# Optimization experiments

Hardware: AMD Instinct MI355X
Metric: run time of the kernel (lower is better)

## Reference

```python
import jax, jax.numpy as jnp
import numpy as np


def ternarize_weight(w):
    # abs-mean threshold quantization to {-am, 0, +am}
    abs_mean = jnp.maximum(jnp.abs(w).mean(), 1e-5)
    thr = 0.7 * abs_mean
    q = jnp.where(w > thr, 1.0, jnp.where(w < -thr, -1.0, 0.0))
    # STE: forward value is q*abs_mean, grad flows to w as identity
    return w + jax.lax.stop_gradient(q * abs_mean - w)


def rotate_half(x):
    x1, x2 = jnp.split(x, 2, axis=-1)
    return jnp.concatenate([-x2, x1], axis=-1)


def setup_inputs() -> dict:
    key = jax.random.key(0)
    k1, k2, k3, k4, k5 = jax.random.split(key, 5)
    B, T, C, H = 2, 2048, 1024, 16
    D = C // H
    x = jax.random.normal(k1, (B, T, C), dtype=jnp.float32)
    cos = jax.random.uniform(k2, (1, 1, T, D), dtype=jnp.float32)
    sin = jax.random.uniform(k3, (1, 1, T, D), dtype=jnp.float32)
    w_qkv = jax.random.normal(k4, (3 * C, C), dtype=jnp.float32) / np.sqrt(C)
    w_proj = jax.random.normal(k5, (C, C), dtype=jnp.float32) / np.sqrt(C)
    return {"x": x, "cos": cos, "sin": sin, "w_qkv": w_qkv, "w_proj": w_proj}


def reference(x, cos, sin, w_qkv, w_proj):
    B, T, C = x.shape
    H = 16
    D = C // H
    wq = ternarize_weight(w_qkv)
    wp = ternarize_weight(w_proj)
    qkv = x @ wq.T  # [B,T,3C]
    q, k, v = jnp.split(qkv, 3, axis=-1)
    # [B,T,C] -> [B,H,T,D]
    q = q.reshape(B, T, H, D).transpose(0, 2, 1, 3)
    k = k.reshape(B, T, H, D).transpose(0, 2, 1, 3)
    v = v.reshape(B, T, H, D).transpose(0, 2, 1, 3)
    # RoPE
    q = q * cos + rotate_half(q) * sin
    k = k * cos + rotate_half(k) * sin
    # causal SDPA
    scale = 1.0 / np.sqrt(D)
    scores = jnp.einsum("bhqd,bhkd->bhqk", q, k) * scale
    causal = jnp.tril(jnp.ones((T, T), dtype=bool))
    scores = jnp.where(causal, scores, jnp.finfo(scores.dtype).min)
    attn = jax.nn.softmax(scores, axis=-1)
    y = jnp.einsum("bhqk,bhkd->bhqd", attn, v)  # [B,H,T,D]
    y = y.transpose(0, 2, 1, 3).reshape(B, T, C)
    return y @ wp.T
```

## Files before the change

### kernel.cpp

```cpp
#include <hip/hip_runtime.h>
#include <hip/hip_bf16.h>

#define B_ 2
#define T_ 2048
#define C_ 1024
#define H_ 16
#define D_ 64
#define M_ 4096
#define N3C 3072

using short8  = __attribute__((ext_vector_type(8))) short;
using floatx4 = __attribute__((ext_vector_type(4))) float;
typedef unsigned int u32;

__device__ __forceinline__ unsigned short f2b(float f) {
  __hip_bfloat16 h = __float2bfloat16(f);
  return *reinterpret_cast<unsigned short*>(&h);
}
__device__ __forceinline__ float b2f(unsigned short u) {
  union { unsigned int i; float f; } x; x.i = ((unsigned int)u) << 16; return x.f;
}
__device__ __forceinline__ u32 pk2(float a, float b) {
  float2 t; t.x = a; t.y = b;
  __hip_bfloat162 p = __float22bfloat162_rn(t);
  return *reinterpret_cast<u32*>(&p);
}

#if __has_builtin(__builtin_amdgcn_exp2f)
__device__ __forceinline__ float ex2(float x) { return __builtin_amdgcn_exp2f(x); }
#else
__device__ __forceinline__ float ex2(float x) { return exp2f(x); }
#endif

__device__ __forceinline__ void gll16(const void* g, void* l) {
  __builtin_amdgcn_global_load_lds((const __attribute__((address_space(1))) u32*)g,
                                   (__attribute__((address_space(3))) u32*)l, 16, 0, 0);
}

#define SYNCV(N) do {                                                   \
    asm volatile("s_waitcnt vmcnt(" #N ")" ::: "memory");               \
    __builtin_amdgcn_s_barrier();                                       \
    asm volatile("" ::: "memory");                                      \
  } while (0)


__global__ void abs_sum2(const float* __restrict__ wq, const float* __restrict__ wp,
                         double* __restrict__ sums) {
  __shared__ double red[4];
  const float* w = blockIdx.y ? wp : wq;
  const int n4 = blockIdx.y ? (C_ * C_ / 4) : (3 * C_ * C_ / 4);
  int stride = gridDim.x * blockDim.x;
  double s = 0.0;
  for (int i = blockIdx.x * blockDim.x + threadIdx.x; i < n4; i += stride) {
    float4 v = ((const float4*)w)[i];
    s += (double)fabsf(v.x) + (double)fabsf(v.y) + (double)fabsf(v.z) + (double)fabsf(v.w);
  }
  #pragma unroll
  for (int off = 32; off > 0; off >>= 1)
    s += __shfl_down(s, off, 64);
  if ((threadIdx.x & 63) == 0) red[threadIdx.x >> 6] = s;
  __syncthreads();
  if (threadIdx.x == 0) atomicAdd(sums + blockIdx.y, (red[0] + red[1]) + (red[2] + red[3]));
}

__global__ void tern_cvt(const float* __restrict__ wq, const float* __restrict__ wp,
                         const float* __restrict__ x,
                         unsigned short* __restrict__ oq, unsigned short* __restrict__ op,
                         unsigned short* __restrict__ xb,
                         const double* __restrict__ sums, float* __restrict__ ams) {
  const int NQ = 3 * C_ * C_;
  const int NP = C_ * C_;
  int i = blockIdx.x * blockDim.x + threadIdx.x;
  float am0 = fmaxf((float)(sums[0] * (1.0 / NQ)), 1e-5f);
  float am1 = fmaxf((float)(sums[1] * (1.0 / NP)), 1e-5f);
  if (i == 0) { ams[0] = am0; ams[1] = am1; }
  if (i < NQ) {
    float thr = 0.7f * am0, v = wq[i];
    oq[i] = (v > thr) ? 0x3F80u : ((v < -thr) ? 0xBF80u : 0u);
  } else if (i < NQ + NP) {
    int j = i - NQ;
    float thr = 0.7f * am1, v = wp[j];
    op[j] = (v > thr) ? 0x3F80u : ((v < -thr) ? 0xBF80u : 0u);
  } else {
    int j = i - NQ - NP;
    float4 v = ((const float4*)x)[j];
    ushort4 o; o.x = f2b(v.x); o.y = f2b(v.y); o.z = f2b(v.z); o.w = f2b(v.w);
    ((ushort4*)xb)[j] = o;
  }
}


__global__ __launch_bounds__(256) void gemm_qkv(const unsigned short* __restrict__ A,
                                                const unsigned short* __restrict__ W,
                                                const float* __restrict__ scale_ptr,
                                                const float* __restrict__ cosp,
                                                const float* __restrict__ sinp,
                                                unsigned short* __restrict__ Qb,
                                                unsigned short* __restrict__ Kb,
                                                unsigned short* __restrict__ Vtb) {
  const int K = C_;
  __shared__ __attribute__((aligned(16))) unsigned short As[3][128 * 32];
  __shared__ __attribute__((aligned(16))) unsigned short Ws[3][192 * 32];
  const int tid = threadIdx.x, lane = tid & 63, wv = tid >> 6;
  const int m = lane & 15, g = lane >> 4;
  const int m0 = blockIdx.y * 128, n0 = blockIdx.x * 192;
  const int wm = (wv >> 1) * 64, wn = wv & 1;

  const int srow16 = lane >> 2;
  const int skoff = (lane & 3) * 8;
  const unsigned short* ga0 = A + (size_t)(m0 + wv * 32 + srow16) * K + skoff;
  const unsigned short* ga1 = A + (size_t)(m0 + wv * 32 + 16 + srow16) * K + skoff;
  const unsigned short* gw0 = W + (size_t)(n0 + (wv + 0) * 16 + srow16) * K + skoff;
  const unsigned short* gw1 = W + (size_t)(n0 + (wv + 4) * 16 + srow16) * K + skoff;
  const unsigned short* gw2 = W + (size_t)(n0 + (wv + 8) * 16 + srow16) * K + skoff;
  const int oA0 = (wv * 32) * 32;
  const int oA1 = (wv * 32 + 16) * 32;
  const int oW0 = ((wv + 0) * 16) * 32;
  const int oW1 = ((wv + 4) * 16) * 32;
  const int oW2 = ((wv + 8) * 16) * 32;

  floatx4 acc[4][6] = {};

#define QSTAGE(T) do {                                                    \
    gll16(ga0, &As[T][oA0]); gll16(ga1, &As[T][oA1]);                     \
    gll16(gw0, &Ws[T][oW0]); gll16(gw1, &Ws[T][oW1]);                     \
    gll16(gw2, &Ws[T][oW2]);                                              \
    ga0 += 32; ga1 += 32; gw0 += 32; gw1 += 32; gw2 += 32;                \
  } while (0)

#define QCOMP(T) do {                                                     \
    short8 af[4], wf[6];                                                  \
    _Pragma("unroll")                                                     \
    for (int r = 0; r < 4; r++)                                           \
      af[r] = *(const short8*)&As[T][(wm + r * 16 + m) * 32 + g * 8];     \
    _Pragma("unroll")                                                     \
    for (int j = 0; j < 6; j++)                                           \
      wf[j] = *(const short8*)&Ws[T][((2 * j + wn) * 16 + m) * 32 + g * 8]; \
    _Pragma("unroll")                                                     \
    for (int r = 0; r < 4; r++)                                           \
      _Pragma("unroll")                                                   \
      for (int j = 0; j < 6; j++)                                         \
        acc[r][j] = __builtin_amdgcn_mfma_f32_16x16x32_bf16(af[r], wf[j], acc[r][j], 0, 0, 0); \
  } while (0)

  QSTAGE(0);
  QSTAGE(1);
  SYNCV(5);
  for (int tt = 0; tt < 10; ++tt) {
    QSTAGE(2); QCOMP(0); SYNCV(5);
    QSTAGE(0); QCOMP(1); SYNCV(5);
    QSTAGE(1); QCOMP(2); SYNCV(5);
  }
  QCOMP(0); SYNCV(0);
  QCOMP(1);
#undef QSTAGE
#undef QCOMP

  const float am = *scale_ptr;
  #pragma unroll
  for (int j = 0; j < 6; j++) {
    const int colb = n0 + (2 * j + wn) * 16;
    const int sect = colb >> 10;
    const int h = (colb >> 6) & 15;
    const int pb = colb & 63;
    const int p = pb + m;
    if (sect < 2) {
      unsigned short* dst = sect ? Kb : Qb;
      const float sc = sect ? am : am * 0.18033688011112042f;
      const bool hi = (pb & 32) != 0;
      #pragma unroll
      for (int r = 0; r < 4; r++)
        #pragma unroll
        for (int i = 0; i < 4; i++) {
          int row = m0 + wm + r * 16 + g * 4 + i;
          int t = row & (T_ - 1), b = row >> 11;
          float cv = cosp[t * 64 + p], sv = sinp[t * 64 + p];
          float a = acc[r][j][i], pt = acc[r][j ^ 1][i];
          float val = hi ? (a * cv + pt * sv) : (a * cv - pt * sv);
          dst[((size_t)(b * H_ + h) * T_ + t) * 64 + p] = f2b(val * sc);
        }
    } else {
      #pragma unroll
      for (int r = 0; r < 4; r++)
        #pragma unroll
        for (int i = 0; i < 4; i++) {
          int row = m0 + wm + r * 16 + g * 4 + i;
          int t = row & (T_ - 1), b = row >> 11;
          size_t hbase = (size_t)(b * H_ + h) * 64 * T_;
          Vtb[hbase + (size_t)p * T_ + t] = f2b(acc[r][j][i] * am);
        }
    }
  }
}


__global__ __launch_bounds__(256) void gemm_proj(const unsigned short* __restrict__ A,
                                                 const unsigned short* __restrict__ W,
                                                 const float* __restrict__ scale_ptr,
                                                 float* __restrict__ Cout) {
  const int K = C_, N = C_;
  __shared__ __attribute__((aligned(16))) unsigned short As[3][128 * 32];
  __shared__ __attribute__((aligned(16))) unsigned short Ws[3][128 * 32];
  const int tid = threadIdx.x, lane = tid & 63, wv = tid >> 6;
  const int m = lane & 15, g = lane >> 4;
  const int m0 = blockIdx.y * 128, n0 = blockIdx.x * 128;
  const int wm = (wv >> 1) * 64, wn = (wv & 1) * 64;

  const int srow16 = lane >> 2;
  const int skoff = (lane & 3) * 8;
  const unsigned short* ga0 = A + (size_t)(m0 + wv * 32 + srow16) * K + skoff;
  const unsigned short* ga1 = A + (size_t)(m0 + wv * 32 + 16 + srow16) * K + skoff;
  const unsigned short* gw0 = W + (size_t)(n0 + wv * 32 + srow16) * K + skoff;
  const unsigned short* gw1 = W + (size_t)(n0 + wv * 32 + 16 + srow16) * K + skoff;
  const int o0 = (wv * 32) * 32;
  const int o1 = (wv * 32 + 16) * 32;

  floatx4 acc[4][4] = {};

#define PSTAGE(T) do {                                                    \
    gll16(ga0, &As[T][o0]); gll16(ga1, &As[T][o1]);                       \
    gll16(gw0, &Ws[T][o0]); gll16(gw1, &Ws[T][o1]);                       \
    ga0 += 32; ga1 += 32; gw0 += 32; gw1 += 32;                           \
  } while (0)

#define PCOMP(T) do {                                                     \
    short8 af[4], wf[4];                                                  \
    _Pragma("unroll")                                                     \
    for (int r = 0; r < 4; r++)                                           \
      af[r] = *(const short8*)&As[T][(wm + r * 16 + m) * 32 + g * 8];     \
    _Pragma("unroll")                                                     \
    for (int c = 0; c < 4; c++)                                           \
      wf[c] = *(const short8*)&Ws[T][(wn + c * 16 + m) * 32 + g * 8];     \
    _Pragma("unroll")                                                     \
    for (int r = 0; r < 4; r++)                                           \
      _Pragma("unroll")                                                   \
      for (int c = 0; c < 4; c++)                                         \
        acc[r][c] = __builtin_amdgcn_mfma_f32_16x16x32_bf16(af[r], wf[c], acc[r][c], 0, 0, 0); \
  } while (0)

  PSTAGE(0);
  PSTAGE(1);
  SYNCV(4);
  for (int tt = 0; tt < 10; ++tt) {
    PSTAGE(2); PCOMP(0); SYNCV(4);
    PSTAGE(0); PCOMP(1); SYNCV(4);
    PSTAGE(1); PCOMP(2); SYNCV(4);
  }
  PCOMP(0); SYNCV(0);
  PCOMP(1);
#undef PSTAGE
#undef PCOMP

  const float scale = *scale_ptr;
  #pragma unroll
  for (int r = 0; r < 4; r++)
    #pragma unroll
    for (int c = 0; c < 4; c++)
      #pragma unroll
      for (int i = 0; i < 4; i++) {
        int row = m0 + wm + r * 16 + g * 4 + i;
        int col = n0 + wn + c * 16 + m;
        Cout[(size_t)row * N + col] = acc[r][c][i] * scale;
      }
}


__global__ __launch_bounds__(256) void flash_mfma(const unsigned short* __restrict__ Qb,
                                                  const unsigned short* __restrict__ Kb,
                                                  const unsigned short* __restrict__ Vtb,
                                                  unsigned short* __restrict__ Y) {
  __shared__ __align__(16) unsigned short Ktile[2][64][64];
  __shared__ __align__(16) unsigned short Vtile[2][64][64];
  __shared__ __align__(16) unsigned short Plds[4][16][72];
  const int lane = threadIdx.x & 63;
  const int wv = threadIdx.x >> 6;
  const int m = lane & 15, g = lane >> 4;
  const int gid = blockIdx.x;
  const int xcd = gid & 7, j = gid >> 3;
  const int bh = xcd * 4 + (j & 3);
  const int s = 31 - (j >> 2);
  const int b = bh >> 4, h = bh & 15;
  const size_t hb = (size_t)bh * T_ * 64;
  const unsigned short* Kbh = Kb + hb;
  const unsigned short* Vbh = Vtb + hb;
  const int r8 = lane >> 3, cc8 = lane & 7;
  const int gcol = ((cc8 ^ r8) << 3);

  const int ntiles = s + 1;
  const int qbase = s * 64 + wv * 16;
  const int q_glob = qbase + m;

  const unsigned short* qp = Qb + hb + (size_t)(qbase + m) * 64 + g * 8;
  short8 qf0 = *(const short8*)qp;
  short8 qf1 = *(const short8*)(qp + 32);

  short8 ones;
  #pragma unroll
  for (int i = 0; i < 8; i++) ones[i] = (short)0x3F80;

  floatx4 O[4] = {};
  floatx4 accl = {};

  #pragma unroll
  for (int cc = 0; cc < 2; cc++) {
    int row = wv * 16 + cc * 8;
    gll16(Kbh + (size_t)(row + r8) * 64 + gcol, &Ktile[0][row][0]);
    gll16(Vbh + (size_t)(row + r8) * T_ + gcol, &Vtile[0][row][0]);
  }

  for (int kt = 0; kt < ntiles; kt++) {
    const int buf = kt & 1;
    const int kb = kt * 64;
    __syncthreads();
    if (kt + 1 < ntiles) {
      const int kb2 = kb + 64;
      #pragma unroll
      for (int cc = 0; cc < 2; cc++) {
        int row = wv * 16 + cc * 8;
        gll16(Kbh + (size_t)(kb2 + row + r8) * 64 + gcol, &Ktile[1 - buf][row][0]);
        gll16(Vbh + (size_t)(row + r8) * T_ + kb2 + gcol, &Vtile[1 - buf][row][0]);
      }
    }
    floatx4 S[4];
    __builtin_amdgcn_s_setprio(1);
    #pragma unroll
    for (int mt = 0; mt < 4; mt++) {
      int row = mt * 16 + m;
      short8 kf0 = *(const short8*)&Ktile[buf][row][(g ^ (m & 7)) << 3];
      short8 kf1 = *(const short8*)&Ktile[buf][row][((g + 4) ^ (m & 7)) << 3];
      floatx4 sv = {};
      sv = __builtin_amdgcn_mfma_f32_16x16x32_bf16(kf0, qf0, sv, 0, 0, 0);
      sv = __builtin_amdgcn_mfma_f32_16x16x32_bf16(kf1, qf1, sv, 0, 0, 0);
      S[mt] = sv;
    }
    __builtin_amdgcn_s_setprio(0);
    if (kt + 1 < ntiles) {
      #pragma unroll
      for (int mt = 0; mt < 4; mt++) {
        uint2 w;
        w.x = pk2(ex2(S[mt][0]), ex2(S[mt][1]));
        w.y = pk2(ex2(S[mt][2]), ex2(S[mt][3]));
        *(uint2*)&Plds[wv][m][mt * 16 + g * 4] = w;
      }
    } else {
      #pragma unroll
      for (int mt = 0; mt < 4; mt++) {
        float e[4];
        #pragma unroll
        for (int r = 0; r < 4; r++) {
          int kg = kb + mt * 16 + g * 4 + r;
          e[r] = (kg <= q_glob) ? ex2(S[mt][r]) : 0.f;
        }
        uint2 w;
        w.x = pk2(e[0], e[1]);
        w.y = pk2(e[2], e[3]);
        *(uint2*)&Plds[wv][m][mt * 16 + g * 4] = w;
      }
    }
    short8 pa0 = *(const short8*)&Plds[wv][m][g * 8];
    short8 pa1 = *(const short8*)&Plds[wv][m][32 + g * 8];
    __builtin_amdgcn_s_setprio(1);
    #pragma unroll
    for (int nt = 0; nt < 4; nt++) {
      int row = nt * 16 + m;
      short8 v0 = *(const short8*)&Vtile[buf][row][(g ^ (m & 7)) << 3];
      short8 v1 = *(const short8*)&Vtile[buf][row][((g + 4) ^ (m & 7)) << 3];
      O[nt] = __builtin_amdgcn_mfma_f32_16x16x32_bf16(pa0, v0, O[nt], 0, 0, 0);
      O[nt] = __builtin_amdgcn_mfma_f32_16x16x32_bf16(pa1, v1, O[nt], 0, 0, 0);
    }
    accl = __builtin_amdgcn_mfma_f32_16x16x32_bf16(pa0, ones, accl, 0, 0, 0);
    accl = __builtin_amdgcn_mfma_f32_16x16x32_bf16(pa1, ones, accl, 0, 0, 0);
    __builtin_amdgcn_s_setprio(0);
  }

  float li[4];
  #pragma unroll
  for (int r = 0; r < 4; r++) li[r] = 1.0f / accl[r];
  #pragma unroll
  for (int nt = 0; nt < 4; nt++)
    #pragma unroll
    for (int r = 0; r < 4; r++) {
      int trow = qbase + g * 4 + r;
      int col = h * 64 + nt * 16 + m;
      Y[(size_t)(b * T_ + trow) * C_ + col] = f2b(O[nt][r] * li[r]);
    }
}


extern "C" void kernel_launch(void* const* d_in, const int* in_sizes, int n_in,
                              void* d_out, int out_size, void* d_ws, size_t ws_size,
                              hipStream_t stream) {
  (void)in_sizes; (void)n_in; (void)out_size; (void)ws_size;
  const float* x      = (const float*)d_in[0];
  const float* cosp   = (const float*)d_in[1];
  const float* sinp   = (const float*)d_in[2];
  const float* w_qkv  = (const float*)d_in[3];
  const float* w_proj = (const float*)d_in[4];
  float* out = (float*)d_out;

  char* ws = (char*)d_ws;
  double* sums = (double*)ws;
  float*  ams  = (float*)(ws + 16);
  unsigned short* wqkv_b  = (unsigned short*)(ws + 256);
  unsigned short* wproj_b = wqkv_b + (size_t)N3C * C_;
  unsigned short* xb      = wproj_b + (size_t)C_ * C_;
  unsigned short* Qb      = xb + (size_t)M_ * C_;
  unsigned short* Kb      = Qb + (size_t)B_ * H_ * T_ * D_;
  unsigned short* Vtb     = Kb + (size_t)B_ * H_ * T_ * D_;
  unsigned short* yb      = Vtb + (size_t)B_ * H_ * T_ * D_;

  hipMemsetAsync(sums, 0, 16, stream);
  abs_sum2<<<dim3(256, 2), 256, 0, stream>>>(w_qkv, w_proj, sums);
  tern_cvt<<<(4 * C_ * C_ + M_ * C_ / 4) / 256, 256, 0, stream>>>(w_qkv, w_proj, x,
                                                                  wqkv_b, wproj_b, xb,
                                                                  sums, ams);
  gemm_qkv<<<dim3(N3C / 192, M_ / 128), 256, 0, stream>>>(xb, wqkv_b, ams + 0,
                                                          cosp, sinp, Qb, Kb, Vtb);
  flash_mfma<<<1024, 256, 0, stream>>>(Qb, Kb, Vtb, yb);
  gemm_proj<<<dim3(C_ / 128, M_ / 128), 256, 0, stream>>>(yb, wproj_b, ams + 1, out);
}
```

Measured before the change: 194.7 us.

## Enlarge QKV GEMM block tile to 256 rows with 8 waves

The QKV projection GEMM now uses 512-thread blocks that each cover 256 rows of M instead of 128, so every staged weight tile is shared by twice as many output rows. Weight tile loading is spread across the 8 waves, with the lower four waves loading one extra chunk, and each wave group waits on its own outstanding-load count before the barrier. This halves the number of blocks and the total weight traffic, at the cost of more shared memory per block and fewer blocks for the scheduler to spread across compute units.

```diff
diff --git a/kernel.cpp b/kernel.cpp
--- a/kernel.cpp
+++ b/kernel.cpp
@@ -90,7 +90,7 @@
 }
 
 
-__global__ __launch_bounds__(256) void gemm_qkv(const unsigned short* __restrict__ A,
+__global__ __launch_bounds__(512) void gemm_qkv(const unsigned short* __restrict__ A,
                                                 const unsigned short* __restrict__ W,
                                                 const float* __restrict__ scale_ptr,
                                                 const float* __restrict__ cosp,
@@ -99,33 +99,39 @@
                                                 unsigned short* __restrict__ Kb,
                                                 unsigned short* __restrict__ Vtb) {
   const int K = C_;
-  __shared__ __attribute__((aligned(16))) unsigned short As[3][128 * 32];
+  __shared__ __attribute__((aligned(16))) unsigned short As[3][256 * 32];
   __shared__ __attribute__((aligned(16))) unsigned short Ws[3][192 * 32];
   const int tid = threadIdx.x, lane = tid & 63, wv = tid >> 6;
   const int m = lane & 15, g = lane >> 4;
-  const int m0 = blockIdx.y * 128, n0 = blockIdx.x * 192;
+  const int m0 = blockIdx.y * 256, n0 = blockIdx.x * 192;
   const int wm = (wv >> 1) * 64, wn = wv & 1;
+  const bool wlow = (wv < 4);
 
   const int srow16 = lane >> 2;
   const int skoff = (lane & 3) * 8;
   const unsigned short* ga0 = A + (size_t)(m0 + wv * 32 + srow16) * K + skoff;
   const unsigned short* ga1 = A + (size_t)(m0 + wv * 32 + 16 + srow16) * K + skoff;
-  const unsigned short* gw0 = W + (size_t)(n0 + (wv + 0) * 16 + srow16) * K + skoff;
-  const unsigned short* gw1 = W + (size_t)(n0 + (wv + 4) * 16 + srow16) * K + skoff;
-  const unsigned short* gw2 = W + (size_t)(n0 + (wv + 8) * 16 + srow16) * K + skoff;
+  const unsigned short* gw0 = W + (size_t)(n0 + wv * 16 + srow16) * K + skoff;
+  const unsigned short* gw1 = W + (size_t)(n0 + 128 + wv * 16 + srow16) * K + skoff;
   const int oA0 = (wv * 32) * 32;
   const int oA1 = (wv * 32 + 16) * 32;
-  const int oW0 = ((wv + 0) * 16) * 32;
-  const int oW1 = ((wv + 4) * 16) * 32;
-  const int oW2 = ((wv + 8) * 16) * 32;
+  const int oW0 = (wv * 16) * 32;
+  const int oW1 = (128 + wv * 16) * 32;
 
   floatx4 acc[4][6] = {};
 
 #define QSTAGE(T) do {                                                    \
     gll16(ga0, &As[T][oA0]); gll16(ga1, &As[T][oA1]);                     \
-    gll16(gw0, &Ws[T][oW0]); gll16(gw1, &Ws[T][oW1]);                     \
-    gll16(gw2, &Ws[T][oW2]);                                              \
-    ga0 += 32; ga1 += 32; gw0 += 32; gw1 += 32; gw2 += 32;                \
+    gll16(gw0, &Ws[T][oW0]);                                              \
+    if (wlow) gll16(gw1, &Ws[T][oW1]);                                    \
+    ga0 += 32; ga1 += 32; gw0 += 32; gw1 += 32;                           \
+  } while (0)
+
+#define QSYNC() do {                                                      \
+    if (wlow) asm volatile("s_waitcnt vmcnt(4)" ::: "memory");            \
+    else      asm volatile("s_waitcnt vmcnt(3)" ::: "memory");            \
+    __builtin_amdgcn_s_barrier();                                         \
+    asm volatile("" ::: "memory");                                        \
   } while (0)
 
 #define QCOMP(T) do {                                                     \
@@ -145,15 +151,16 @@
 
   QSTAGE(0);
   QSTAGE(1);
-  SYNCV(5);
+  QSYNC();
   for (int tt = 0; tt < 10; ++tt) {
-    QSTAGE(2); QCOMP(0); SYNCV(5);
-    QSTAGE(0); QCOMP(1); SYNCV(5);
-    QSTAGE(1); QCOMP(2); SYNCV(5);
+    QSTAGE(2); QCOMP(0); QSYNC();
+    QSTAGE(0); QCOMP(1); QSYNC();
+    QSTAGE(1); QCOMP(2); QSYNC();
   }
   QCOMP(0); SYNCV(0);
   QCOMP(1);
 #undef QSTAGE
+#undef QSYNC
 #undef QCOMP
 
   const float am = *scale_ptr;
@@ -414,7 +421,7 @@
   tern_cvt<<<(4 * C_ * C_ + M_ * C_ / 4) / 256, 256, 0, stream>>>(w_qkv, w_proj, x,
                                                                   wqkv_b, wproj_b, xb,
                                                                   sums, ams);
-  gemm_qkv<<<dim3(N3C / 192, M_ / 128), 256, 0, stream>>>(xb, wqkv_b, ams + 0,
+  gemm_qkv<<<dim3(N3C / 192, M_ / 256), 512, 0, stream>>>(xb, wqkv_b, ams + 0,
                                                           cosp, sinp, Qb, Kb, Vtb);
   flash_mfma<<<1024, 256, 0, stream>>>(Qb, Kb, Vtb, yb);
   gemm_proj<<<dim3(C_ / 128, M_ / 128), 256, 0, stream>>>(yb, wproj_b, ams + 1, out);
```

Result: slower. 201.8 us (+3.6%).
